# Performance work log

Measured on AMD Instinct MI355X. Metric: run time of the kernel, lower is better.

## Reference

```python
import jax, jax.numpy as jnp
import numpy as np

NUM_EXPERTS = 64


def setup_inputs() -> dict:
    key = jax.random.key(0)
    k1, k2 = jax.random.split(key)
    x = jax.random.normal(k1, (4, 4096, 2048), dtype=jnp.float32)
    # nn.Linear default init scale ~ 1/sqrt(dim); exact init irrelevant for correctness
    gate_w = jax.random.normal(k2, (NUM_EXPERTS, 2048), dtype=jnp.float32) * (1.0 / np.sqrt(2048.0))
    expert_bias = jnp.zeros((NUM_EXPERTS,), dtype=jnp.float32)
    return {"x": x, "gate_w": gate_w, "expert_bias": expert_bias, "top_k": 8}


def reference(x, gate_w, expert_bias, top_k):
    # x: [B, S, D]; gate_w: [E, D]; expert_bias: [E]
    B, S, D = x.shape
    x_flat = x.reshape(-1, D)                                  # [T, D], T = B*S
    logits = jnp.einsum('td,ed->te', x_flat, gate_w) + expert_bias  # [T, E]
    top_k_logits, top_k_indices = jax.lax.top_k(logits, top_k)      # [T, K]
    top_k_weights = jax.nn.softmax(top_k_logits, axis=-1)           # [T, K]
    # training-mode load counting (scatter_add over expert ids)
    expert_counts = jax.ops.segment_sum(
        jnp.ones((B * S * top_k,), dtype=jnp.float32),
        top_k_indices.reshape(-1),
        num_segments=NUM_EXPERTS,
    )                                                               # [E]
    return top_k_indices, top_k_weights, expert_counts
```

## Files before the change

kernel.cpp:

```cpp
#include <hip/hip_runtime.h>
#include <math.h>

#define T_TOKENS 16384
#define D_DIM    2048
#define E_EXP    64
#define TOPK     8
#define NS       4
#define KC       32
#define NCH      (D_DIM / NS / KC)
#define TT       32
#define TOKP     36

typedef __attribute__((ext_vector_type(8))) short bf16x8;
typedef __attribute__((ext_vector_type(4))) float f32x4;

__device__ __forceinline__ unsigned short bf16rne(float f) {
  unsigned u = __builtin_bit_cast(unsigned, f);
  unsigned r = u + 0x7fffu + ((u >> 16) & 1u);
  return (unsigned short)(r >> 16);
}
__device__ __forceinline__ float bf16f(unsigned short h) {
  return __builtin_bit_cast(float, (unsigned)h << 16);
}

__device__ __forceinline__ void gload16(const void* g, void* l) {
  __builtin_amdgcn_global_load_lds(
      (const __attribute__((address_space(1))) unsigned int*)g,
      (__attribute__((address_space(3))) unsigned int*)l,
      16, 0, 0);
}

__global__ __launch_bounds__(256) void convert_g_kernel(
    const float* __restrict__ gw, unsigned short* __restrict__ ph,
    unsigned short* __restrict__ pl, float* __restrict__ counts_zero)
{
  const int id = blockIdx.x * 256 + threadIdx.x;
  if (blockIdx.x == 0 && threadIdx.x < E_EXP) counts_zero[threadIdx.x] = 0.0f;

  const int e  = id & 63;
  const int kq = (id >> 6) & 3;
  const int c  = id >> 8;
  const float* gp = &gw[(size_t)e * D_DIM + c * 32 + kq * 8];
  float4 v0 = *(const float4*)&gp[0];
  float4 v1 = *(const float4*)&gp[4];
  const float xs[8] = {v0.x, v0.y, v0.z, v0.w, v1.x, v1.y, v1.z, v1.w};
  bf16x8 hi, lo;
  #pragma unroll
  for (int j = 0; j < 8; ++j) {
    unsigned short h = bf16rne(xs[j]);
    hi[j] = (short)h;
    lo[j] = (short)bf16rne(xs[j] - bf16f(h));
  }
  *(bf16x8*)&ph[(size_t)id * 8] = hi;
  *(bf16x8*)&pl[(size_t)id * 8] = lo;
}

__global__ __launch_bounds__(512, 4) void moe_fused_kernel(
    const float* __restrict__ x, const unsigned short* __restrict__ ph,
    const unsigned short* __restrict__ pl, const float* __restrict__ bias,
    float* __restrict__ out)
{
  __shared__ char smem[49152];
  __shared__ unsigned hist[E_EXP];

  const int tid  = threadIdx.x;
  const int wave = tid >> 6;
  const int lane = tid & 63;
  const int l15  = lane & 15;
  const int quad = lane >> 4;
  const int wg   = wave & 1;
  const int wsl  = wave >> 1;
  const int tok0 = blockIdx.x * TT;
  const int tokw = tok0 + wg * 16;

  const int jA0 = wave * 2;
  const int jA1 = wave * 2 + 1;
  const int aslot = ((lane & 7) ^ ((lane >> 3) & 7)) * 4;
  const float* gA0 = &x[(size_t)(tok0 + (jA0 & 3) * 8 + (lane >> 3)) * D_DIM
                        + (jA0 >> 2) * (D_DIM / NS) + aslot];
  const float* gA1 = &x[(size_t)(tok0 + (jA1 & 3) * 8 + (lane >> 3)) * D_DIM
                        + (jA1 >> 2) * (D_DIM / NS) + aslot];
  const int mB = wave * 4;
  const unsigned short* gB[4];
  #pragma unroll
  for (int i = 0; i < 4; ++i) {
    const int m = mB + i;
    const unsigned short* base = ((m >> 2) & 1) ? pl : ph;
    gB[i] = base + ((size_t)((m >> 3) * NCH)) * 2048 + (m & 3) * 512 + lane * 8;
  }

#define STAGE(c)                                                           \
  {                                                                        \
    gload16(gA0 + (size_t)(c) * KC, (void*)(smem + jA0 * 1024));           \
    gload16(gA1 + (size_t)(c) * KC, (void*)(smem + jA1 * 1024));           \
    gload16(gB[0] + (size_t)(c) * 2048, (void*)(smem + 16384 + (mB+0)*1024)); \
    gload16(gB[1] + (size_t)(c) * 2048, (void*)(smem + 16384 + (mB+1)*1024)); \
    gload16(gB[2] + (size_t)(c) * 2048, (void*)(smem + 16384 + (mB+2)*1024)); \
    gload16(gB[3] + (size_t)(c) * 2048, (void*)(smem + 16384 + (mB+3)*1024)); \
  }

  f32x4 acc[4];
  #pragma unroll
  for (int et = 0; et < 4; ++et) acc[et] = (f32x4){0.f, 0.f, 0.f, 0.f};

  const float* aRow = (const float*)smem + ((wsl * 32 + wg * 16 + l15) * 32);
  const int ps0 = ((quad * 2)     ^ (l15 & 7)) * 4;
  const int ps1 = ((quad * 2 + 1) ^ (l15 & 7)) * 4;
  const unsigned short* bq = (const unsigned short*)(smem + 16384)
                             + wsl * 4096 + quad * 512 + l15 * 8;

  STAGE(0);
  __syncthreads();

  #pragma unroll 1
  for (int c = 0; c < NCH; ++c) {
    f32x4 a0 = *(const f32x4*)&aRow[ps0];
    f32x4 a1 = *(const f32x4*)&aRow[ps1];

    bf16x8 bh[4], bl[4];
    #pragma unroll
    for (int et = 0; et < 4; ++et) {
      bh[et] = *(const bf16x8*)&bq[et * 128];
      bl[et] = *(const bf16x8*)&bq[2048 + et * 128];
    }

    const float xs[8] = {a0[0], a0[1], a0[2], a0[3], a1[0], a1[1], a1[2], a1[3]};
    bf16x8 ah, al;
    #pragma unroll
    for (int j = 0; j < 8; ++j) {
      unsigned short h = bf16rne(xs[j]);
      ah[j] = (short)h;
      al[j] = (short)bf16rne(xs[j] - bf16f(h));
    }

    #pragma unroll
    for (int et = 0; et < 4; ++et) {
      acc[et] = __builtin_amdgcn_mfma_f32_16x16x32_bf16(ah, bh[et], acc[et], 0, 0, 0);
      acc[et] = __builtin_amdgcn_mfma_f32_16x16x32_bf16(al, bh[et], acc[et], 0, 0, 0);
      acc[et] = __builtin_amdgcn_mfma_f32_16x16x32_bf16(ah, bl[et], acc[et], 0, 0, 0);
    }

    __syncthreads();
    if (c + 1 < NCH) {
      STAGE(c + 1);
      __syncthreads();
    }
  }

  float* slab = (float*)smem;

  #pragma unroll
  for (int et = 0; et < 4; ++et) {
    *(f32x4*)&slab[((size_t)(wsl * E_EXP + et * 16 + l15)) * TOKP + wg * 16 + quad * 4] = acc[et];
  }
  if (tid < E_EXP) hist[tid] = 0;
  __syncthreads();

  {
    const int e  = tid >> 3;
    const int t4 = (tid & 7) * 4;
    f32x4 s0 = *(const f32x4*)&slab[(size_t)(0 * E_EXP + e) * TOKP + t4];
    f32x4 s1 = *(const f32x4*)&slab[(size_t)(1 * E_EXP + e) * TOKP + t4];
    f32x4 s2 = *(const f32x4*)&slab[(size_t)(2 * E_EXP + e) * TOKP + t4];
    f32x4 s3 = *(const f32x4*)&slab[(size_t)(3 * E_EXP + e) * TOKP + t4];
    const float b = bias[e];
    f32x4 v;
    #pragma unroll
    for (int j = 0; j < 4; ++j) v[j] = (((b + s0[j]) + s1[j]) + s2[j]) + s3[j];
    *(f32x4*)&slab[(size_t)(0 * E_EXP + e) * TOKP + t4] = v;
  }
  __syncthreads();

  if (tid >= 64) return;

  if (tid < TT) {
    const int t = tid;
    float l[E_EXP];
    #pragma unroll
    for (int j = 0; j < E_EXP; ++j) l[j] = slab[(size_t)j * TOKP + t];

    float tv[TOPK]; int tix[TOPK];
    unsigned long long used = 0ull;
    #pragma unroll
    for (int k = 0; k < TOPK; ++k) {
      float best = -INFINITY; int bi = 0;
      #pragma unroll
      for (int j = 0; j < E_EXP; ++j) {
        bool ok = (((used >> j) & 1ull) == 0ull) && (l[j] > best);
        best = ok ? l[j] : best;
        bi   = ok ? j : bi;
      }
      tv[k] = best; tix[k] = bi;
      used |= (1ull << bi);
    }

    float m = tv[0], s = 0.0f, w[TOPK];
    #pragma unroll
    for (int k = 0; k < TOPK; ++k) { w[k] = expf(tv[k] - m); s += w[k]; }
    float inv = 1.0f / s;

    const size_t gt = (size_t)blockIdx.x * TT + t;
    #pragma unroll
    for (int k = 0; k < TOPK; ++k) {
      out[gt * TOPK + k] = (float)tix[k];
      out[(size_t)T_TOKENS * TOPK + gt * TOPK + k] = w[k] * inv;
    }

    #pragma unroll
    for (int k = 0; k < TOPK; ++k) atomicAdd(&hist[tix[k]], 1u);
  }
  __threadfence_block();
  atomicAdd(&out[2 * (size_t)T_TOKENS * TOPK + tid], (float)hist[tid]);
}

extern "C" void kernel_launch(void* const* d_in, const int* in_sizes, int n_in,
                              void* d_out, int out_size, void* d_ws, size_t ws_size,
                              hipStream_t stream) {
  const float* x    = (const float*)d_in[0];
  const float* gw   = (const float*)d_in[1];
  const float* bias = (const float*)d_in[2];
  float* out  = (float*)d_out;

  unsigned short* ph = (unsigned short*)d_ws;
  unsigned short* pl = ph + (size_t)E_EXP * D_DIM;

  convert_g_kernel<<<dim3(E_EXP * D_DIM / 8 / 256), dim3(256), 0, stream>>>(
      gw, ph, pl, out + 2 * (size_t)T_TOKENS * TOPK);
  moe_fused_kernel<<<dim3(T_TOKENS / TT), dim3(512), 0, stream>>>(
      x, ph, pl, bias, out);
}
```

Measured before the change: 214.1 us.

## Double-buffer x tiles in LDS and load gate weights directly from global

The main loop now stages 256-wide K panels of x into two 32KB LDS buffers and prefetches the next panel while computing the current one, so there is one barrier per panel instead of two per 32-wide chunk. The bf16 hi/lo gate weights are no longer staged through LDS. Each wave reads its fragments straight from global memory into registers, relying on the cache since all blocks share them. The trade is more LDS per block (64KB), which may lower occupancy below the launch-bounds target, plus extra register pressure from holding two sub-chunks of B fragments.

```diff
diff --git a/kernel.cpp b/kernel.cpp
--- a/kernel.cpp
+++ b/kernel.cpp
@@ -6,8 +6,8 @@
 #define E_EXP    64
 #define TOPK     8
 #define NS       4
-#define KC       32
-#define NCH      (D_DIM / NS / KC)
+#define PH       8
+#define PKC      256
 #define TT       32
 #define TOKP     36
 
@@ -60,7 +60,7 @@
     const unsigned short* __restrict__ pl, const float* __restrict__ bias,
     float* __restrict__ out)
 {
-  __shared__ char smem[49152];
+  __shared__ char smem[65536];
   __shared__ unsigned hist[E_EXP];
 
   const int tid  = threadIdx.x;
@@ -71,80 +71,78 @@
   const int wg   = wave & 1;
   const int wsl  = wave >> 1;
   const int tok0 = blockIdx.x * TT;
-  const int tokw = tok0 + wg * 16;
-
-  const int jA0 = wave * 2;
-  const int jA1 = wave * 2 + 1;
-  const int aslot = ((lane & 7) ^ ((lane >> 3) & 7)) * 4;
-  const float* gA0 = &x[(size_t)(tok0 + (jA0 & 3) * 8 + (lane >> 3)) * D_DIM
-                        + (jA0 >> 2) * (D_DIM / NS) + aslot];
-  const float* gA1 = &x[(size_t)(tok0 + (jA1 & 3) * 8 + (lane >> 3)) * D_DIM
-                        + (jA1 >> 2) * (D_DIM / NS) + aslot];
-  const int mB = wave * 4;
-  const unsigned short* gB[4];
+
+  const int srow = wave * 4;
+  const float* gS[4];
   #pragma unroll
   for (int i = 0; i < 4; ++i) {
-    const int m = mB + i;
-    const unsigned short* base = ((m >> 2) & 1) ? pl : ph;
-    gB[i] = base + ((size_t)((m >> 3) * NCH)) * 2048 + (m & 3) * 512 + lane * 8;
-  }
-
-#define STAGE(c)                                                           \
+    const int row = srow + i;
+    gS[i] = &x[(size_t)(tok0 + row) * D_DIM + (size_t)(lane ^ (row & 7)) * 4];
+  }
+
+#define STAGE(p, buf)                                                      \
   {                                                                        \
-    gload16(gA0 + (size_t)(c) * KC, (void*)(smem + jA0 * 1024));           \
-    gload16(gA1 + (size_t)(c) * KC, (void*)(smem + jA1 * 1024));           \
-    gload16(gB[0] + (size_t)(c) * 2048, (void*)(smem + 16384 + (mB+0)*1024)); \
-    gload16(gB[1] + (size_t)(c) * 2048, (void*)(smem + 16384 + (mB+1)*1024)); \
-    gload16(gB[2] + (size_t)(c) * 2048, (void*)(smem + 16384 + (mB+2)*1024)); \
-    gload16(gB[3] + (size_t)(c) * 2048, (void*)(smem + 16384 + (mB+3)*1024)); \
-  }
+    gload16(gS[0] + (size_t)(p) * PKC, (void*)(smem + (buf) * 32768 + (srow + 0) * 1024)); \
+    gload16(gS[1] + (size_t)(p) * PKC, (void*)(smem + (buf) * 32768 + (srow + 1) * 1024)); \
+    gload16(gS[2] + (size_t)(p) * PKC, (void*)(smem + (buf) * 32768 + (srow + 2) * 1024)); \
+    gload16(gS[3] + (size_t)(p) * PKC, (void*)(smem + (buf) * 32768 + (srow + 3) * 1024)); \
+  }
+
+  const unsigned short* bh0 = ph + quad * 512 + l15 * 8;
+  const unsigned short* bl0 = pl + quad * 512 + l15 * 8;
 
   f32x4 acc[4];
   #pragma unroll
   for (int et = 0; et < 4; ++et) acc[et] = (f32x4){0.f, 0.f, 0.f, 0.f};
 
-  const float* aRow = (const float*)smem + ((wsl * 32 + wg * 16 + l15) * 32);
-  const int ps0 = ((quad * 2)     ^ (l15 & 7)) * 4;
-  const int ps1 = ((quad * 2 + 1) ^ (l15 & 7)) * 4;
-  const unsigned short* bq = (const unsigned short*)(smem + 16384)
-                             + wsl * 4096 + quad * 512 + l15 * 8;
-
-  STAGE(0);
+  const int swk = l15 & 7;
+
+  STAGE(0, 0);
   __syncthreads();
 
+  int buf = 0;
   #pragma unroll 1
-  for (int c = 0; c < NCH; ++c) {
-    f32x4 a0 = *(const f32x4*)&aRow[ps0];
-    f32x4 a1 = *(const f32x4*)&aRow[ps1];
-
-    bf16x8 bh[4], bl[4];
-    #pragma unroll
-    for (int et = 0; et < 4; ++et) {
-      bh[et] = *(const bf16x8*)&bq[et * 128];
-      bl[et] = *(const bf16x8*)&bq[2048 + et * 128];
-    }
-
-    const float xs[8] = {a0[0], a0[1], a0[2], a0[3], a1[0], a1[1], a1[2], a1[3]};
-    bf16x8 ah, al;
-    #pragma unroll
-    for (int j = 0; j < 8; ++j) {
-      unsigned short h = bf16rne(xs[j]);
-      ah[j] = (short)h;
-      al[j] = (short)bf16rne(xs[j] - bf16f(h));
-    }
-
-    #pragma unroll
-    for (int et = 0; et < 4; ++et) {
-      acc[et] = __builtin_amdgcn_mfma_f32_16x16x32_bf16(ah, bh[et], acc[et], 0, 0, 0);
-      acc[et] = __builtin_amdgcn_mfma_f32_16x16x32_bf16(al, bh[et], acc[et], 0, 0, 0);
-      acc[et] = __builtin_amdgcn_mfma_f32_16x16x32_bf16(ah, bl[et], acc[et], 0, 0, 0);
+  for (int p = 0; p < PH; ++p) {
+    bf16x8 bh[2][4], bl[2][4];
+    #pragma unroll
+    for (int sub = 0; sub < 2; ++sub) {
+      const size_t cg = (size_t)(p * 8 + wsl * 2 + sub) * 2048;
+      #pragma unroll
+      for (int et = 0; et < 4; ++et) {
+        bh[sub][et] = *(const bf16x8*)&bh0[cg + et * 128];
+        bl[sub][et] = *(const bf16x8*)&bl0[cg + et * 128];
+      }
+    }
+
+    if (p + 1 < PH) STAGE(p + 1, buf ^ 1);
+
+    const float* ab = (const float*)(smem + buf * 32768) + (wg * 16 + l15) * 256;
+
+    #pragma unroll
+    for (int sub = 0; sub < 2; ++sub) {
+      const int s0 = wsl * 16 + sub * 8 + quad * 2;
+      f32x4 a0 = *(const f32x4*)&ab[((s0    ) ^ swk) * 4];
+      f32x4 a1 = *(const f32x4*)&ab[((s0 + 1) ^ swk) * 4];
+
+      const float xs[8] = {a0[0], a0[1], a0[2], a0[3], a1[0], a1[1], a1[2], a1[3]};
+      bf16x8 ah, al;
+      #pragma unroll
+      for (int j = 0; j < 8; ++j) {
+        unsigned short h = bf16rne(xs[j]);
+        ah[j] = (short)h;
+        al[j] = (short)bf16rne(xs[j] - bf16f(h));
+      }
+
+      #pragma unroll
+      for (int et = 0; et < 4; ++et) {
+        acc[et] = __builtin_amdgcn_mfma_f32_16x16x32_bf16(ah, bh[sub][et], acc[et], 0, 0, 0);
+        acc[et] = __builtin_amdgcn_mfma_f32_16x16x32_bf16(al, bh[sub][et], acc[et], 0, 0, 0);
+        acc[et] = __builtin_amdgcn_mfma_f32_16x16x32_bf16(ah, bl[sub][et], acc[et], 0, 0, 0);
+      }
     }
 
     __syncthreads();
-    if (c + 1 < NCH) {
-      STAGE(c + 1);
-      __syncthreads();
-    }
+    buf ^= 1;
   }
 
   float* slab = (float*)smem;
```

Result: no change. 212.9 us (-0.5%).
